# Performance work log

Measured on AMD Instinct MI355X. Metric: run time of the kernel, lower is better.

## Reference

```python
import jax, jax.numpy as jnp
import numpy as np

B, S, D = 8, 8192, 1024
FILTER_SIZE = 4


def setup_inputs() -> dict:
    key = jax.random.key(0)
    k1, k2, k3 = jax.random.split(key, 3)
    x = jax.random.normal(k1, (B, S, D), dtype=jnp.float32)
    # projection to [bias, filter_size coefficients]
    W = jax.random.normal(k2, (D, FILTER_SIZE + 1), dtype=jnp.float32) / np.sqrt(D)
    noise = jax.random.uniform(k3, (B, S, 1), dtype=jnp.float32)
    return {"x": x, "W": W, "noise": noise}


def reference(x, W, noise):
    """Sequentially-dependent gater.
    gate_logits[i] = log p(g_i=1 | g_{<i}), gate_probs[i] = p, gate_samples[i] ~ Bernoulli(p).
    Filter weights are a linear projection of x; the per-step logit is
    bias + <coeffs, last filter_size samples> (zeros before t=0).
    Returns (gate_logits, gate_probs, gate_samples), each [B, S, 1].
    """
    b, s, d = x.shape
    fsz = W.shape[1] - 1
    # precompute_filter_weights: [B, S, 1+filter_size]
    fw = jnp.einsum('bsd,df->bsf', x, W)

    def step(window, inputs):
        # window: [B, fsz] most recent samples, oldest first
        fw_t, u_t = inputs  # [B, 1+fsz], [B]
        logit = fw_t[:, 0] + jnp.sum(window * fw_t[:, 1:], axis=-1)  # [B]
        logp = jax.nn.log_sigmoid(logit)
        p = jax.nn.sigmoid(logit)
        samp = (u_t < p).astype(x.dtype)
        new_window = jnp.concatenate([window[:, 1:], samp[:, None]], axis=1)
        return new_window, (logp, p, samp)

    window0 = jnp.zeros((b, fsz), dtype=x.dtype)
    xs = (jnp.swapaxes(fw, 0, 1), jnp.swapaxes(noise[..., 0], 0, 1))  # [S, B, ...]
    _, (logps, ps, samps) = jax.lax.scan(step, window0, xs)

    to_out = lambda a: jnp.swapaxes(a, 0, 1)[..., None]  # [S,B] -> [B,S,1]
    return to_out(logps), to_out(ps), to_out(samps)
```

## Files before the change

### kernel.cpp

```cpp
#include <hip/hip_runtime.h>
#include <cstdint>
#include <cstddef>


namespace {

constexpr int kB = 8;
constexpr int kS = 8192;
constexpr int kD = 1024;
constexpr int kRows = kB * kS;
constexpr int kT = 16;
constexpr int kCPB = kS / kT;
constexpr int kChunks = kB * kCPB;
constexpr int kRPW = 32;
constexpr unsigned long long kIdMap = 0xFEDCBA9876543210ull;

__device__ __forceinline__ float logit_from_state(unsigned int w,
                                                  const float4& A,
                                                  const float4& Bv) {
  const float s1 = (w & 1u) ? A.y : 0.0f;
  const float s2 = (w & 2u) ? A.z : 0.0f;
  const float s3 = (w & 4u) ? A.w : 0.0f;
  const float s4 = (w & 8u) ? Bv.x : 0.0f;
  return A.x + (((s1 + s2) + s3) + s4);
}

__device__ __forceinline__ unsigned long long compose(unsigned long long a,
                                                      unsigned long long b) {
  unsigned long long r = 0;
#pragma unroll
  for (int s = 0; s < 16; ++s) {
    const unsigned int e = (unsigned int)(a >> (4 * s)) & 15u;
    r |= ((b >> (4 * e)) & 15ull) << (4 * s);
  }
  return r;
}

}

__global__ __launch_bounds__(256, 2) void proj_map_kernel(
    const float* __restrict__ x, const float* __restrict__ W,
    const float* __restrict__ noise, float* __restrict__ fwu,
    unsigned int* __restrict__ trajbuf, unsigned long long* __restrict__ maps) {
  __shared__ float Wl[kD * 5];
  __shared__ float fl[4][kT * 8];
  const int tid = threadIdx.x;
  const int lane = tid & 63;
  const int wv = tid >> 6;
  const int wid = blockIdx.x * 4 + wv;
  const int r0 = wid * kRPW;

  float nu = 0.5f, nth = 0.0f;
  if (lane < kRPW) nu = noise[r0 + lane];

  const float4* W4 = reinterpret_cast<const float4*>(W);
  float4* Wl4 = reinterpret_cast<float4*>(Wl);
#pragma unroll
  for (int i = 0; i < 5; ++i) Wl4[tid + 256 * i] = W4[tid + 256 * i];

  if (lane < kRPW) nth = logf(nu / (1.0f - nu));
  __syncthreads();

  float wr[4][4][5];
#pragma unroll
  for (int j = 0; j < 4; ++j)
#pragma unroll
    for (int k = 0; k < 4; ++k) {
      const int d = j * 256 + lane * 4 + k;
#pragma unroll
      for (int f = 0; f < 5; ++f) wr[j][k][f] = Wl[d * 5 + f];
    }

  auto prefetch_row = [&](float4(&v)[4], int t) {
    if (t < kRPW) {
      const float4* xp =
          reinterpret_cast<const float4*>(x + (size_t)(r0 + t) * kD);
#pragma unroll
      for (int j = 0; j < 4; ++j) v[j] = xp[j * 64 + lane];
    }
  };

  auto do_row = [&](const float4(&v)[4], int t) {
    float acc[5] = {0.f, 0.f, 0.f, 0.f, 0.f};
#pragma unroll
    for (int j = 0; j < 4; ++j) {
      const float e[4] = {v[j].x, v[j].y, v[j].z, v[j].w};
#pragma unroll
      for (int k = 0; k < 4; ++k)
#pragma unroll
        for (int f = 0; f < 5; ++f) acc[f] += e[k] * wr[j][k][f];
    }
#pragma unroll
    for (int off = 32; off >= 1; off >>= 1)
#pragma unroll
      for (int f = 0; f < 5; ++f) acc[f] += __shfl_xor(acc[f], off);

    const float u = __shfl(nu, t);
    const float th = __shfl(nth, t);
    if (lane == 0) {
      const float4 o0 = make_float4(acc[0], acc[1], acc[2], acc[3]);
      const float4 o1 = make_float4(acc[4], u, th, 0.0f);
      float4* og = reinterpret_cast<float4*>(fwu + (size_t)(r0 + t) * 8);
      og[0] = o0;
      og[1] = o1;
      float4* ol = reinterpret_cast<float4*>(&fl[wv][(t & 15) * 8]);
      ol[0] = o0;
      ol[1] = o1;
    }
  };

  auto sim = [&](int c) {
    unsigned int cur = (unsigned int)(lane & 15);
    unsigned int traj = 0;
#pragma unroll
    for (int i = 0; i < kT; ++i) {
      const float4* p = reinterpret_cast<const float4*>(&fl[wv][i * 8]);
      const float4 A = p[0];
      const float4 Bv = p[1];
      const unsigned int d = (logit_from_state(cur, A, Bv) > Bv.z) ? 1u : 0u;
      traj |= d << i;
      cur = (cur >> 1) | (d << 3);
    }
    if (lane < 16) trajbuf[(size_t)c * 16 + lane] = traj;
    const unsigned long long b0 = __ballot((int)(cur & 1u));
    const unsigned long long b1 = __ballot((int)(cur & 2u));
    const unsigned long long b2 = __ballot((int)(cur & 4u));
    const unsigned long long b3 = __ballot((int)(cur & 8u));
    if (lane == 0) {
      unsigned long long m = 0;
#pragma unroll
      for (int s = 0; s < 16; ++s) {
        const unsigned long long e =
            ((b0 >> s) & 1ull) | (((b1 >> s) & 1ull) << 1) |
            (((b2 >> s) & 1ull) << 2) | (((b3 >> s) & 1ull) << 3);
        m |= e << (4 * s);
      }
      maps[c] = m;
    }
  };

  float4 va[4], vb[4];
  prefetch_row(va, 0);
  prefetch_row(vb, 1);
#pragma unroll 1
  for (int tp = 0; tp < 16; ++tp) {
    do_row(va, 2 * tp);
    prefetch_row(va, 2 * tp + 2);
    do_row(vb, 2 * tp + 1);
    prefetch_row(vb, 2 * tp + 3);
    if (tp == 7) sim(wid * 2);
    if (tp == 15) sim(wid * 2 + 1);
  }
}

__global__ __launch_bounds__(256) void scan_emit_kernel(
    const float* __restrict__ fwu, const unsigned long long* __restrict__ maps,
    const unsigned int* __restrict__ trajbuf, float* __restrict__ out) {
  __shared__ unsigned char starts_lds[kCPB];
  const int tid = threadIdx.x;
  const int lane = tid & 63;
  const int wv = tid >> 6;
  const int bid = blockIdx.x;
  const int b = bid >> 5;
  const int row = bid * 256 + tid;

  const float4* p = reinterpret_cast<const float4*>(fwu + (size_t)row * 8);
  const float4 A = p[0];
  const float4 Bv = p[1];

  if (wv == 0) {
    unsigned long long m[8];
    const unsigned long long* mb = maps + b * kCPB + lane * 8;
#pragma unroll
    for (int i = 0; i < 8; ++i) m[i] = mb[i];
    unsigned long long c = m[0];
#pragma unroll
    for (int i = 1; i < 8; ++i) c = compose(c, m[i]);
    unsigned long long scan = c;
#pragma unroll
    for (int off = 1; off < 64; off <<= 1) {
      const unsigned long long prev = __shfl_up(scan, off);
      if (lane >= off) scan = compose(prev, scan);
    }
    unsigned long long pref = __shfl_up(scan, 1);
    if (lane == 0) pref = kIdMap;
    unsigned int s = (unsigned int)(pref & 15ull);
#pragma unroll
    for (int i = 0; i < 8; ++i) {
      starts_lds[lane * 8 + i] = (unsigned char)s;
      s = (unsigned int)((m[i] >> (4 * s)) & 15ull);
    }
  }
  __syncthreads();

  const int scl = (row & (kS - 1)) >> 4;
  const int scg = row >> 4;
  const unsigned int st = (unsigned int)starts_lds[scl];
  const unsigned int traj = trajbuf[(size_t)scg * 16 + st];
  const int i = row & 15;
  unsigned int w;
  if (i >= 4)
    w = (traj >> (i - 4)) & 15u;
  else
    w = ((st >> i) | (traj << (4 - i))) & 15u;

  const float logit = logit_from_state(w, A, Bv);
  const float pr = 1.0f / (1.0f + expf(-logit));
  const float lp = fminf(logit, 0.0f) - log1pf(expf(-fabsf(logit)));
  out[row] = lp;
  out[kRows + row] = pr;
  out[2 * kRows + row] = (float)((traj >> i) & 1u);
}

extern "C" void kernel_launch(void* const* d_in, const int* in_sizes, int n_in,
                              void* d_out, int out_size, void* d_ws,
                              size_t ws_size, hipStream_t stream) {
  const float* x = (const float*)d_in[0];
  const float* W = (const float*)d_in[1];
  const float* noise = (const float*)d_in[2];
  float* out = (float*)d_out;

  float* fwu = (float*)d_ws;
  unsigned int* trajbuf =
      (unsigned int*)((char*)d_ws + (size_t)kRows * 8 * sizeof(float));
  unsigned long long* maps =
      (unsigned long long*)((char*)trajbuf +
                            (size_t)kChunks * 16 * sizeof(unsigned int));

  proj_map_kernel<<<512, 256, 0, stream>>>(x, W, noise, fwu, trajbuf, maps);
  scan_emit_kernel<<<kRows / 256, 256, 0, stream>>>(fwu, maps, trajbuf, out);
}
```

Before: 55.19 us.

## Halve rows per wave, double grid, add nontemporal x loads and coalesced fwu store

Each wave of the projection kernel now handles a single 16-row chunk instead of two, so the grid doubles to kChunks/4 blocks and the launch bound asks for three blocks per CU. Loads of x use nontemporal builtins, and the fwu rows are staged in LDS and written with one coalesced store per wave after the chunk simulation, replacing per-row stores from lane 0. The aim is more parallelism and latency hiding for the bandwidth-bound pass over x. The cost is that every wave now reloads the 20 KB W into LDS and registers for half as many rows, so that setup is amortised over less work and register pressure under the tighter launch bound may spill.

```diff
diff --git a/kernel.cpp b/kernel.cpp
--- a/kernel.cpp
+++ b/kernel.cpp
@@ -12,8 +12,9 @@
 constexpr int kT = 16;
 constexpr int kCPB = kS / kT;
 constexpr int kChunks = kB * kCPB;
-constexpr int kRPW = 32;
 constexpr unsigned long long kIdMap = 0xFEDCBA9876543210ull;
+
+typedef float f32x4 __attribute__((ext_vector_type(4)));
 
 __device__ __forceinline__ float logit_from_state(unsigned int w,
                                                   const float4& A,
@@ -38,7 +39,7 @@
 
 }
 
-__global__ __launch_bounds__(256, 2) void proj_map_kernel(
+__global__ __launch_bounds__(256, 3) void proj_map_kernel(
     const float* __restrict__ x, const float* __restrict__ W,
     const float* __restrict__ noise, float* __restrict__ fwu,
     unsigned int* __restrict__ trajbuf, unsigned long long* __restrict__ maps) {
@@ -48,17 +49,17 @@
   const int lane = tid & 63;
   const int wv = tid >> 6;
   const int wid = blockIdx.x * 4 + wv;
-  const int r0 = wid * kRPW;
+  const int r0 = wid * kT;
 
   float nu = 0.5f, nth = 0.0f;
-  if (lane < kRPW) nu = noise[r0 + lane];
+  if (lane < kT) nu = noise[r0 + lane];
 
   const float4* W4 = reinterpret_cast<const float4*>(W);
   float4* Wl4 = reinterpret_cast<float4*>(Wl);
 #pragma unroll
   for (int i = 0; i < 5; ++i) Wl4[tid + 256 * i] = W4[tid + 256 * i];
 
-  if (lane < kRPW) nth = logf(nu / (1.0f - nu));
+  if (lane < kT) nth = logf(nu / (1.0f - nu));
   __syncthreads();
 
   float wr[4][4][5];
@@ -72,11 +73,14 @@
     }
 
   auto prefetch_row = [&](float4(&v)[4], int t) {
-    if (t < kRPW) {
-      const float4* xp =
-          reinterpret_cast<const float4*>(x + (size_t)(r0 + t) * kD);
-#pragma unroll
-      for (int j = 0; j < 4; ++j) v[j] = xp[j * 64 + lane];
+    if (t < kT) {
+      const f32x4* xp =
+          reinterpret_cast<const f32x4*>(x + (size_t)(r0 + t) * kD);
+#pragma unroll
+      for (int j = 0; j < 4; ++j) {
+        const f32x4 q = __builtin_nontemporal_load(xp + j * 64 + lane);
+        v[j] = make_float4(q.x, q.y, q.z, q.w);
+      }
     }
   };
 
@@ -98,18 +102,24 @@
     const float u = __shfl(nu, t);
     const float th = __shfl(nth, t);
     if (lane == 0) {
-      const float4 o0 = make_float4(acc[0], acc[1], acc[2], acc[3]);
-      const float4 o1 = make_float4(acc[4], u, th, 0.0f);
-      float4* og = reinterpret_cast<float4*>(fwu + (size_t)(r0 + t) * 8);
-      og[0] = o0;
-      og[1] = o1;
-      float4* ol = reinterpret_cast<float4*>(&fl[wv][(t & 15) * 8]);
-      ol[0] = o0;
-      ol[1] = o1;
+      float4* ol = reinterpret_cast<float4*>(&fl[wv][t * 8]);
+      ol[0] = make_float4(acc[0], acc[1], acc[2], acc[3]);
+      ol[1] = make_float4(acc[4], u, th, 0.0f);
     }
   };
 
-  auto sim = [&](int c) {
+  float4 va[4], vb[4];
+  prefetch_row(va, 0);
+  prefetch_row(vb, 1);
+#pragma unroll 1
+  for (int tp = 0; tp < 8; ++tp) {
+    do_row(va, 2 * tp);
+    prefetch_row(va, 2 * tp + 2);
+    do_row(vb, 2 * tp + 1);
+    prefetch_row(vb, 2 * tp + 3);
+  }
+
+  {
     unsigned int cur = (unsigned int)(lane & 15);
     unsigned int traj = 0;
 #pragma unroll
@@ -121,7 +131,7 @@
       traj |= d << i;
       cur = (cur >> 1) | (d << 3);
     }
-    if (lane < 16) trajbuf[(size_t)c * 16 + lane] = traj;
+    if (lane < 16) trajbuf[(size_t)wid * 16 + lane] = traj;
     const unsigned long long b0 = __ballot((int)(cur & 1u));
     const unsigned long long b1 = __ballot((int)(cur & 2u));
     const unsigned long long b2 = __ballot((int)(cur & 4u));
@@ -135,21 +145,13 @@
             (((b2 >> s) & 1ull) << 2) | (((b3 >> s) & 1ull) << 3);
         m |= e << (4 * s);
       }
-      maps[c] = m;
-    }
-  };
-
-  float4 va[4], vb[4];
-  prefetch_row(va, 0);
-  prefetch_row(vb, 1);
-#pragma unroll 1
-  for (int tp = 0; tp < 16; ++tp) {
-    do_row(va, 2 * tp);
-    prefetch_row(va, 2 * tp + 2);
-    do_row(vb, 2 * tp + 1);
-    prefetch_row(vb, 2 * tp + 3);
-    if (tp == 7) sim(wid * 2);
-    if (tp == 15) sim(wid * 2 + 1);
+      maps[wid] = m;
+    }
+  }
+
+  if (lane < 32) {
+    const float4 v = reinterpret_cast<const float4*>(&fl[wv][0])[lane];
+    reinterpret_cast<float4*>(fwu + (size_t)r0 * 8)[lane] = v;
   }
 }
 
@@ -227,6 +229,7 @@
       (unsigned long long*)((char*)trajbuf +
                             (size_t)kChunks * 16 * sizeof(unsigned int));
 
-  proj_map_kernel<<<512, 256, 0, stream>>>(x, W, noise, fwu, trajbuf, maps);
+  proj_map_kernel<<<kChunks / 4, 256, 0, stream>>>(x, W, noise, fwu, trajbuf,
+                                                   maps);
   scan_emit_kernel<<<kRows / 256, 256, 0, stream>>>(fwu, maps, trajbuf, out);
 }
```

Measured after the change: 64.67 us. +17.2%, slower.
